# Optimization experiments

Hardware: AMD Instinct MI355X
Metric: run time of the kernel (lower is better)

The kernel has to match this reference:

```python
import jax, jax.numpy as jnp
import numpy as np

B, C, N = 8, 256, 4096
K = C // 4  # projection dim for F and G (feat_dim // 4)


def setup_inputs() -> dict:
    key = jax.random.key(0)
    k1, k2, k3, k4, k5, k6 = jax.random.split(key, 6)
    inp = {
        "input": jax.random.normal(k1, (B, C, N), dtype=jnp.float32),
        "nms_feat": jax.random.normal(k2, (B, C, N), dtype=jnp.float32),
        "WF": jax.random.normal(k3, (K, C), dtype=jnp.float32) * (1.0 / np.sqrt(C)),
        "WG": jax.random.normal(k4, (K, C), dtype=jnp.float32) * (1.0 / np.sqrt(C)),
        "WH": jax.random.normal(k5, (C, C), dtype=jnp.float32) * (1.0 / np.sqrt(C)),
        "gamma": jax.random.normal(k6, (1,), dtype=jnp.float32),
    }
    return inp


def reference(input, nms_feat, WF, WG, WH, gamma):
    feat = nms_feat  # [B, C, N]; module uses nms_feat when provided
    b, c, n = feat.shape
    # 1x1 conv projections == channel matmuls; outputs laid out as [B, N, d]
    f = jnp.einsum('kc,bcn->bnk', WF, feat)   # [B, N, K]
    g = jnp.einsum('kc,bcn->bnk', WG, feat)   # [B, N, K]
    h = jnp.einsum('dc,bcn->bnd', WH, feat)   # [B, N, C]
    # attention scores (no scaling in original module)
    s = jnp.einsum('bnk,bmk->bnm', g, f)      # [B, N, N]
    beta = jax.nn.softmax(s, axis=-1)
    o = jnp.einsum('bnm,bmd->bnd', beta, h)   # [B, N, C]
    # NOTE: the original does a raw reshape [B,N,C] -> [B,C,N] (not a transpose);
    # we reproduce that exactly.
    o = o.reshape(b, c, n)
    return gamma * o + input
```

## Files before the change

kernel.cpp:

```cpp
#include <hip/hip_runtime.h>
#include <hip/hip_bf16.h>

#define BB 8
#define CC 256
#define NN 4096
#define KP 64
#define LOG2E 1.44269504088896f

typedef _Float16 f16x8 __attribute__((ext_vector_type(8)));
typedef _Float16 f16x4 __attribute__((ext_vector_type(4)));
typedef float    f32x4 __attribute__((ext_vector_type(4)));

#define MFMA16(a, b, c) __builtin_amdgcn_mfma_f32_16x16x32_f16((a), (b), (c), 0, 0, 0)

__device__ __forceinline__ float fast_exp2(float x) {
#if __has_builtin(__builtin_amdgcn_exp2f)
    return __builtin_amdgcn_exp2f(x);
#else
    return __expf(x * 0.69314718055994531f);
#endif
}

template<int CTRL>
__device__ __forceinline__ float dpp_ror_f(float x) {
    return __int_as_float(__builtin_amdgcn_update_dpp(
        0, __float_as_int(x), CTRL, 0xF, 0xF, true));
}
__device__ __forceinline__ float max16(float x) {
    x = fmaxf(x, dpp_ror_f<0x128>(x));
    x = fmaxf(x, dpp_ror_f<0x124>(x));
    x = fmaxf(x, dpp_ror_f<0x122>(x));
    x = fmaxf(x, dpp_ror_f<0x121>(x));
    return x;
}
__device__ __forceinline__ float sum16(float x) {
    x += dpp_ror_f<0x128>(x);
    x += dpp_ror_f<0x124>(x);
    x += dpp_ror_f<0x122>(x);
    x += dpp_ror_f<0x121>(x);
    return x;
}

__global__ __launch_bounds__(256) void wconv_kernel(
    const float* __restrict__ WF, const float* __restrict__ WG,
    const float* __restrict__ WH, _Float16* __restrict__ W16)
{
    int gid = blockIdx.x * 256 + threadIdx.x;
    int i4  = gid * 4;
    const float* src;
    if (i4 < 64 * CC)        src = WF + i4;
    else if (i4 < 128 * CC)  src = WG + (i4 - 64 * CC);
    else                     src = WH + (i4 - 128 * CC);
    float4 v = *(const float4*)src;
    f16x4 o = { (_Float16)v.x, (_Float16)v.y, (_Float16)v.z, (_Float16)v.w };
    *(f16x4*)(W16 + i4) = o;
}

__global__ __launch_bounds__(256, 3) void proj16_kernel(
    const float* __restrict__ feat, const _Float16* __restrict__ W16,
    _Float16* __restrict__ fb, _Float16* __restrict__ gb,
    _Float16* __restrict__ hT)
{
    __shared__ __align__(16) _Float16 ft[64][264];
    const int b = blockIdx.y, n0 = blockIdx.x * 64, t = threadIdx.x;

    #pragma unroll
    for (int i = 0; i < 16; i++) {
        int v = t + i * 256, c = v >> 4, nq = v & 15;
        float4 x = *(const float4*)(feat + ((size_t)b * CC + c) * NN + n0 + nq * 4);
        ft[nq * 4 + 0][c] = (_Float16)x.x;
        ft[nq * 4 + 1][c] = (_Float16)x.y;
        ft[nq * 4 + 2][c] = (_Float16)x.z;
        ft[nq * 4 + 3][c] = (_Float16)x.w;
    }
    __syncthreads();

    const int w = t >> 6, lane = t & 63, quad = lane >> 4, ln = lane & 15;
    const int rowbase = w * 96;

    f32x4 acc[6][4] = {};
    #pragma unroll
    for (int ks = 0; ks < 8; ks++) {
        const int c0 = ks * 32;
        f16x8 bfr[4];
        #pragma unroll
        for (int tf = 0; tf < 4; tf++)
            bfr[tf] = *(const f16x8*)&ft[tf * 16 + ln][c0 + quad * 8];
        #pragma unroll
        for (int af = 0; af < 6; af++) {
            f16x8 a = *(const f16x8*)(W16 + (size_t)(rowbase + af * 16 + ln) * CC + c0 + quad * 8);
            #pragma unroll
            for (int tf = 0; tf < 4; tf++)
                acc[af][tf] = MFMA16(a, bfr[tf], acc[af][tf]);
        }
    }

    #pragma unroll
    for (int af = 0; af < 6; af++) {
        const int orow0 = rowbase + af * 16 + quad * 4;
        if (orow0 < 64) {
            #pragma unroll
            for (int tf = 0; tf < 4; tf++) {
                const int tok = n0 + tf * 16 + ln;
                f16x4 pk = { (_Float16)acc[af][tf][0], (_Float16)acc[af][tf][1],
                             (_Float16)acc[af][tf][2], (_Float16)acc[af][tf][3] };
                *(f16x4*)(fb + ((size_t)b * NN + tok) * KP + orow0) = pk;
            }
        } else if (orow0 < 128) {
            #pragma unroll
            for (int tf = 0; tf < 4; tf++) {
                const int tok = n0 + tf * 16 + ln;
                f16x4 pk = { (_Float16)(acc[af][tf][0] * LOG2E),
                             (_Float16)(acc[af][tf][1] * LOG2E),
                             (_Float16)(acc[af][tf][2] * LOG2E),
                             (_Float16)(acc[af][tf][3] * LOG2E) };
                *(f16x4*)(gb + ((size_t)b * NN + tok) * KP + (orow0 - 64)) = pk;
            }
        } else {
            #pragma unroll
            for (int r = 0; r < 4; r++) {
                const int d = orow0 - 128 + r;
                f16x4 pk = { (_Float16)acc[af][0][r], (_Float16)acc[af][1][r],
                             (_Float16)acc[af][2][r], (_Float16)acc[af][3][r] };
                *(f16x4*)(hT + ((size_t)b * CC + d) * NN + n0 + ln * 4) = pk;
            }
        }
    }
}

__global__ __launch_bounds__(256, 2) void attn16_kernel(
    const _Float16* __restrict__ fb, const _Float16* __restrict__ gb,
    const _Float16* __restrict__ hT, const float* __restrict__ inp,
    const float* __restrict__ gamma, float* __restrict__ out)
{
    __shared__ __align__(16) _Float16 g_s[64][72];
    __shared__ __align__(16) _Float16 f_s[64][72];
    __shared__ __align__(16) _Float16 p_s[64][72];
    __shared__ float alpha_s[64];
    __shared__ float l_s[64];

    const int b = blockIdx.x, q0 = blockIdx.y * 64, t = threadIdx.x;
    const int w = t >> 6, lane = t & 63, quad = lane >> 4, ln = lane & 15;
    const int row = t >> 2, kq = t & 3;
    const int dbase = w * 64;

    {
        const _Float16* src = gb + ((size_t)b * NN + q0 + row) * KP + kq * 16;
        *(f16x8*)&g_s[row][kq * 16]     = *(const f16x8*)(src);
        *(f16x8*)&g_s[row][kq * 16 + 8] = *(const f16x8*)(src + 8);
    }
    f16x8 fr0, fr1;
    {
        const _Float16* src = fb + ((size_t)b * NN + row) * KP + kq * 16;
        fr0 = *(const f16x8*)(src);
        fr1 = *(const f16x8*)(src + 8);
    }
    __syncthreads();

    f16x8 ag[2];
    ag[0] = *(const f16x8*)&g_s[w * 16 + ln][quad * 8];
    ag[1] = *(const f16x8*)&g_s[w * 16 + ln][32 + quad * 8];

    float m_run[4] = {-1e30f, -1e30f, -1e30f, -1e30f};
    float l_run[4] = {0.f, 0.f, 0.f, 0.f};
    f32x4 acc[4][4] = {};
    f16x8 hv[2][4];

    #pragma unroll 1
    for (int mt = 0; mt < NN / 64; mt++) {
        const int m0 = mt * 64;

        *(f16x8*)&f_s[row][kq * 16]     = fr0;
        *(f16x8*)&f_s[row][kq * 16 + 8] = fr1;
        __syncthreads();

        {
            const int m0n = ((mt + 1) & 63) * 64;
            const _Float16* srcf = fb + ((size_t)b * NN + m0n + row) * KP + kq * 16;
            fr0 = *(const f16x8*)(srcf);
            fr1 = *(const f16x8*)(srcf + 8);
            #pragma unroll
            for (int ks = 0; ks < 2; ks++)
                #pragma unroll
                for (int df = 0; df < 4; df++)
                    hv[ks][df] = *(const f16x8*)(hT +
                        ((size_t)b * CC + dbase + df * 16 + ln) * NN + m0 + ks * 32 + quad * 8);
        }

        f32x4 S[4] = {};
        #pragma unroll
        for (int ks = 0; ks < 2; ks++) {
            #pragma unroll
            for (int mf = 0; mf < 4; mf++) {
                f16x8 bf = *(const f16x8*)&f_s[mf * 16 + ln][ks * 32 + quad * 8];
                S[mf] = MFMA16(ag[ks], bf, S[mf]);
            }
        }

        #pragma unroll
        for (int r = 0; r < 4; r++) {
            float mx = fmaxf(fmaxf(S[0][r], S[1][r]), fmaxf(S[2][r], S[3][r]));
            mx = max16(mx);
            float mnew = fmaxf(m_run[r], mx);
            float al   = fast_exp2(m_run[r] - mnew);
            float p0 = fast_exp2(S[0][r] - mnew);
            float p1 = fast_exp2(S[1][r] - mnew);
            float p2 = fast_exp2(S[2][r] - mnew);
            float p3 = fast_exp2(S[3][r] - mnew);
            float sum = sum16((p0 + p1) + (p2 + p3));
            l_run[r] = l_run[r] * al + sum;
            m_run[r] = mnew;
            const int qrow = w * 16 + quad * 4 + r;
            if (ln == 0) alpha_s[qrow] = al;
            f16x4 pk = { (_Float16)p0, (_Float16)p1, (_Float16)p2, (_Float16)p3 };
            *(f16x4*)&p_s[qrow][ln * 4] = pk;
        }
        __syncthreads();

        float al_[4][4];
        bool need = false;
        #pragma unroll
        for (int qf = 0; qf < 4; qf++)
            #pragma unroll
            for (int r = 0; r < 4; r++) {
                al_[qf][r] = alpha_s[qf * 16 + quad * 4 + r];
                need |= (al_[qf][r] != 1.0f);
            }
        if (__ballot(need)) {
            #pragma unroll
            for (int qf = 0; qf < 4; qf++)
                #pragma unroll
                for (int df = 0; df < 4; df++)
                    #pragma unroll
                    for (int r = 0; r < 4; r++)
                        acc[qf][df][r] *= al_[qf][r];
        }

        #pragma unroll
        for (int ks = 0; ks < 2; ks++) {
            #pragma unroll
            for (int qf = 0; qf < 4; qf++) {
                f16x8 ap = *(const f16x8*)&p_s[qf * 16 + ln][ks * 32 + quad * 8];
                #pragma unroll
                for (int df = 0; df < 4; df++)
                    acc[qf][df] = MFMA16(ap, hv[ks][df], acc[qf][df]);
            }
        }
    }

    if (ln == 0) {
        #pragma unroll
        for (int r = 0; r < 4; r++) l_s[w * 16 + quad * 4 + r] = l_run[r];
    }
    __syncthreads();

    const float gam = gamma[0];
    #pragma unroll
    for (int qf = 0; qf < 4; qf++) {
        #pragma unroll
        for (int r = 0; r < 4; r++) {
            const int q = qf * 16 + quad * 4 + r;
            const float linv = 1.0f / l_s[q];
            #pragma unroll
            for (int df = 0; df < 4; df++) {
                const int d = dbase + df * 16 + ln;
                size_t idx = ((size_t)b * NN + q0 + q) * CC + d;
                out[idx] = fmaf(gam, acc[qf][df][r] * linv, inp[idx]);
            }
        }
    }
}

extern "C" void kernel_launch(void* const* d_in, const int* in_sizes, int n_in,
                              void* d_out, int out_size, void* d_ws, size_t ws_size,
                              hipStream_t stream) {
    const float* input = (const float*)d_in[0];
    const float* nms   = (const float*)d_in[1];
    const float* WF    = (const float*)d_in[2];
    const float* WG    = (const float*)d_in[3];
    const float* WH    = (const float*)d_in[4];
    const float* gamma = (const float*)d_in[5];
    float* out = (float*)d_out;

    char* ws = (char*)d_ws;
    _Float16* W16  = (_Float16*)ws;
    _Float16* fb16 = (_Float16*)(ws + 196608);
    _Float16* gb16 = (_Float16*)(ws + 196608 + 4194304);
    _Float16* hT16 = (_Float16*)(ws + 196608 + 2 * 4194304);

    wconv_kernel<<<96, 256, 0, stream>>>(WF, WG, WH, W16);
    proj16_kernel<<<dim3(NN / 64, BB), 256, 0, stream>>>(nms, W16, fb16, gb16, hT16);
    attn16_kernel<<<dim3(BB, NN / 64), 256, 0, stream>>>(fb16, gb16, hT16, input, gamma, out);
}
```

Baseline: 255.7 us.

## Double-buffer attention tiles, use lazy max rescaling, defer row-sum reduction

Double-buffers the F tile, P tile and alpha arrays in shared memory and prefetches the H registers one tile ahead. This removes one of the two block barriers per key tile and gives global loads more time to land. The online-softmax max is only refreshed when a wave sees a score exceed the running max by a threshold, which skips most rescale passes. The per-row sum reduction is moved out of the loop to a single final shuffle. The cost is higher register and LDS use, and exponent values can grow up to 2^10 before rescaling, which risks fp16 range and precision in the P values.

```diff
diff --git a/kernel.cpp b/kernel.cpp
--- a/kernel.cpp
+++ b/kernel.cpp
@@ -134,9 +134,10 @@
     const float* __restrict__ gamma, float* __restrict__ out)
 {
     __shared__ __align__(16) _Float16 g_s[64][72];
-    __shared__ __align__(16) _Float16 f_s[64][72];
-    __shared__ __align__(16) _Float16 p_s[64][72];
-    __shared__ float alpha_s[64];
+    __shared__ __align__(16) _Float16 f_s[2][64][72];
+    __shared__ __align__(16) _Float16 p_s[2][64][72];
+    __shared__ float alpha_s[2][64];
+    __shared__ float chg_s[2][4];
     __shared__ float l_s[64];
 
     const int b = blockIdx.x, q0 = blockIdx.y * 64, t = threadIdx.x;
@@ -161,96 +162,122 @@
     ag[0] = *(const f16x8*)&g_s[w * 16 + ln][quad * 8];
     ag[1] = *(const f16x8*)&g_s[w * 16 + ln][32 + quad * 8];
 
+    *(f16x8*)&f_s[0][row][kq * 16]     = fr0;
+    *(f16x8*)&f_s[0][row][kq * 16 + 8] = fr1;
+
+    f16x8 hvA[2][4], hvB[2][4];
+    #pragma unroll
+    for (int ks = 0; ks < 2; ks++)
+        #pragma unroll
+        for (int df = 0; df < 4; df++)
+            hvA[ks][df] = *(const f16x8*)(hT +
+                ((size_t)b * CC + dbase + df * 16 + ln) * NN + ks * 32 + quad * 8);
+    {
+        const _Float16* src = fb + ((size_t)b * NN + 64 + row) * KP + kq * 16;
+        fr0 = *(const f16x8*)(src);
+        fr1 = *(const f16x8*)(src + 8);
+    }
+    __syncthreads();
+
     float m_run[4] = {-1e30f, -1e30f, -1e30f, -1e30f};
     float l_run[4] = {0.f, 0.f, 0.f, 0.f};
     f32x4 acc[4][4] = {};
-    f16x8 hv[2][4];
+
+#define ATTN_PHASE(CUR, NXT, HVC, HVN, MT)                                     \
+    {                                                                          \
+        f32x4 S[4] = {};                                                       \
+        _Pragma("unroll")                                                      \
+        for (int ks = 0; ks < 2; ks++) {                                       \
+            _Pragma("unroll")                                                  \
+            for (int mf = 0; mf < 4; mf++) {                                   \
+                f16x8 bf = *(const f16x8*)&f_s[CUR][mf * 16 + ln][ks * 32 + quad * 8]; \
+                S[mf] = MFMA16(ag[ks], bf, S[mf]);                             \
+            }                                                                  \
+        }                                                                      \
+        float pmax[4]; bool upd = false;                                       \
+        _Pragma("unroll")                                                      \
+        for (int r = 0; r < 4; r++) {                                          \
+            pmax[r] = fmaxf(fmaxf(S[0][r], S[1][r]), fmaxf(S[2][r], S[3][r])); \
+            upd |= (pmax[r] > m_run[r] + 10.0f);                               \
+        }                                                                      \
+        const bool wave_upd = (__ballot(upd) != 0ull);                         \
+        if (wave_upd) {                                                        \
+            _Pragma("unroll")                                                  \
+            for (int r = 0; r < 4; r++) {                                      \
+                float mx   = max16(pmax[r]);                                   \
+                float mnew = fmaxf(m_run[r], mx);                              \
+                float al   = fast_exp2(m_run[r] - mnew);                       \
+                l_run[r] *= al;                                                \
+                m_run[r]  = mnew;                                              \
+                if (ln == 0) alpha_s[CUR][w * 16 + quad * 4 + r] = al;         \
+            }                                                                  \
+        }                                                                      \
+        if (lane == 0) chg_s[CUR][w] = wave_upd ? 1.0f : 0.0f;                 \
+        _Pragma("unroll")                                                      \
+        for (int r = 0; r < 4; r++) {                                          \
+            float p0 = fast_exp2(S[0][r] - m_run[r]);                          \
+            float p1 = fast_exp2(S[1][r] - m_run[r]);                          \
+            float p2 = fast_exp2(S[2][r] - m_run[r]);                          \
+            float p3 = fast_exp2(S[3][r] - m_run[r]);                          \
+            l_run[r] += (p0 + p1) + (p2 + p3);                                 \
+            f16x4 pk = { (_Float16)p0, (_Float16)p1, (_Float16)p2, (_Float16)p3 }; \
+            *(f16x4*)&p_s[CUR][w * 16 + quad * 4 + r][ln * 4] = pk;            \
+        }                                                                      \
+        *(f16x8*)&f_s[NXT][row][kq * 16]     = fr0;                            \
+        *(f16x8*)&f_s[NXT][row][kq * 16 + 8] = fr1;                            \
+        __syncthreads();                                                       \
+        {                                                                      \
+            const int m0n = (((MT) + 1) & 63) * 64;                            \
+            _Pragma("unroll")                                                  \
+            for (int ks = 0; ks < 2; ks++)                                     \
+                _Pragma("unroll")                                              \
+                for (int df = 0; df < 4; df++)                                 \
+                    HVN[ks][df] = *(const f16x8*)(hT +                         \
+                        ((size_t)b * CC + dbase + df * 16 + ln) * NN + m0n + ks * 32 + quad * 8); \
+            const int m0n2 = (((MT) + 2) & 63) * 64;                           \
+            const _Float16* srcf = fb + ((size_t)b * NN + m0n2 + row) * KP + kq * 16; \
+            fr0 = *(const f16x8*)(srcf);                                       \
+            fr1 = *(const f16x8*)(srcf + 8);                                   \
+        }                                                                      \
+        {                                                                      \
+            float chg[4] = { chg_s[CUR][0], chg_s[CUR][1],                     \
+                             chg_s[CUR][2], chg_s[CUR][3] };                   \
+            _Pragma("unroll")                                                  \
+            for (int qf = 0; qf < 4; qf++) {                                   \
+                if (chg[qf] != 0.0f) {                                         \
+                    _Pragma("unroll")                                          \
+                    for (int r = 0; r < 4; r++) {                              \
+                        float al = alpha_s[CUR][qf * 16 + quad * 4 + r];       \
+                        _Pragma("unroll")                                      \
+                        for (int df = 0; df < 4; df++)                         \
+                            acc[qf][df][r] *= al;                              \
+                    }                                                          \
+                }                                                              \
+            }                                                                  \
+        }                                                                      \
+        _Pragma("unroll")                                                      \
+        for (int ks = 0; ks < 2; ks++) {                                       \
+            _Pragma("unroll")                                                  \
+            for (int qf = 0; qf < 4; qf++) {                                   \
+                f16x8 ap = *(const f16x8*)&p_s[CUR][qf * 16 + ln][ks * 32 + quad * 8]; \
+                _Pragma("unroll")                                              \
+                for (int df = 0; df < 4; df++)                                 \
+                    acc[qf][df] = MFMA16(ap, HVC[ks][df], acc[qf][df]);        \
+            }                                                                  \
+        }                                                                      \
+    }
 
     #pragma unroll 1
-    for (int mt = 0; mt < NN / 64; mt++) {
-        const int m0 = mt * 64;
-
-        *(f16x8*)&f_s[row][kq * 16]     = fr0;
-        *(f16x8*)&f_s[row][kq * 16 + 8] = fr1;
-        __syncthreads();
-
-        {
-            const int m0n = ((mt + 1) & 63) * 64;
-            const _Float16* srcf = fb + ((size_t)b * NN + m0n + row) * KP + kq * 16;
-            fr0 = *(const f16x8*)(srcf);
-            fr1 = *(const f16x8*)(srcf + 8);
-            #pragma unroll
-            for (int ks = 0; ks < 2; ks++)
-                #pragma unroll
-                for (int df = 0; df < 4; df++)
-                    hv[ks][df] = *(const f16x8*)(hT +
-                        ((size_t)b * CC + dbase + df * 16 + ln) * NN + m0 + ks * 32 + quad * 8);
-        }
-
-        f32x4 S[4] = {};
-        #pragma unroll
-        for (int ks = 0; ks < 2; ks++) {
-            #pragma unroll
-            for (int mf = 0; mf < 4; mf++) {
-                f16x8 bf = *(const f16x8*)&f_s[mf * 16 + ln][ks * 32 + quad * 8];
-                S[mf] = MFMA16(ag[ks], bf, S[mf]);
-            }
-        }
-
-        #pragma unroll
-        for (int r = 0; r < 4; r++) {
-            float mx = fmaxf(fmaxf(S[0][r], S[1][r]), fmaxf(S[2][r], S[3][r]));
-            mx = max16(mx);
-            float mnew = fmaxf(m_run[r], mx);
-            float al   = fast_exp2(m_run[r] - mnew);
-            float p0 = fast_exp2(S[0][r] - mnew);
-            float p1 = fast_exp2(S[1][r] - mnew);
-            float p2 = fast_exp2(S[2][r] - mnew);
-            float p3 = fast_exp2(S[3][r] - mnew);
-            float sum = sum16((p0 + p1) + (p2 + p3));
-            l_run[r] = l_run[r] * al + sum;
-            m_run[r] = mnew;
-            const int qrow = w * 16 + quad * 4 + r;
-            if (ln == 0) alpha_s[qrow] = al;
-            f16x4 pk = { (_Float16)p0, (_Float16)p1, (_Float16)p2, (_Float16)p3 };
-            *(f16x4*)&p_s[qrow][ln * 4] = pk;
-        }
-        __syncthreads();
-
-        float al_[4][4];
-        bool need = false;
-        #pragma unroll
-        for (int qf = 0; qf < 4; qf++)
-            #pragma unroll
-            for (int r = 0; r < 4; r++) {
-                al_[qf][r] = alpha_s[qf * 16 + quad * 4 + r];
-                need |= (al_[qf][r] != 1.0f);
-            }
-        if (__ballot(need)) {
-            #pragma unroll
-            for (int qf = 0; qf < 4; qf++)
-                #pragma unroll
-                for (int df = 0; df < 4; df++)
-                    #pragma unroll
-                    for (int r = 0; r < 4; r++)
-                        acc[qf][df][r] *= al_[qf][r];
-        }
-
-        #pragma unroll
-        for (int ks = 0; ks < 2; ks++) {
-            #pragma unroll
-            for (int qf = 0; qf < 4; qf++) {
-                f16x8 ap = *(const f16x8*)&p_s[qf * 16 + ln][ks * 32 + quad * 8];
-                #pragma unroll
-                for (int df = 0; df < 4; df++)
-                    acc[qf][df] = MFMA16(ap, hv[ks][df], acc[qf][df]);
-            }
-        }
-    }
-
-    if (ln == 0) {
-        #pragma unroll
-        for (int r = 0; r < 4; r++) l_s[w * 16 + quad * 4 + r] = l_run[r];
+    for (int mt2 = 0; mt2 < NN / 128; mt2++) {
+        ATTN_PHASE(0, 1, hvA, hvB, mt2 * 2)
+        ATTN_PHASE(1, 0, hvB, hvA, mt2 * 2 + 1)
+    }
+#undef ATTN_PHASE
+
+    #pragma unroll
+    for (int r = 0; r < 4; r++) {
+        float lt = sum16(l_run[r]);
+        if (ln == 0) l_s[w * 16 + quad * 4 + r] = lt;
     }
     __syncthreads();
 
```

Result: slower. 264.8 us (+3.6%).
